# Kernel optimization log

Hardware: AMD Instinct MI355X
Metric: run time of the kernel (lower is better)

The kernel has to match this reference:

```python
import jax, jax.numpy as jnp
import numpy as np

B, T, DIM = 1, 1024, 1024
H = 8
QLR, KVLR = 768, 512
DNOPE, DROPE, DV = 128, 64, 128
DK = DNOPE + DROPE  # 192
EPS = 1e-5


def _rms(x, w):
    return x * jax.lax.rsqrt(jnp.mean(x * x, axis=-1, keepdims=True) + EPS) * w


def _l2norm(x):
    return x * jax.lax.rsqrt(jnp.sum(x * x, axis=-1, keepdims=True) + 1e-6)


def setup_inputs() -> dict:
    key = jax.random.key(0)
    ks = jax.random.split(key, 12)
    std = 0.02
    rnd = lambda k, shape: (jax.random.normal(k, shape, dtype=jnp.float32) * std)
    return {
        'x': jax.random.normal(ks[0], (B, T, DIM), dtype=jnp.float32),
        'cos': jax.random.normal(ks[1], (T, DROPE), dtype=jnp.float32),
        'sin': jax.random.normal(ks[2], (T, DROPE), dtype=jnp.float32),
        'wq_a': rnd(ks[3], (DIM, QLR)),
        'q_norm_w': jnp.ones((QLR,), dtype=jnp.float32),
        'wq_b': rnd(ks[4], (QLR, H * DK)),
        'wkv_a': rnd(ks[5], (DIM, KVLR + DROPE)),
        'kv_norm_w': jnp.ones((KVLR,), dtype=jnp.float32),
        'wkv_b': rnd(ks[6], (KVLR, H * (DNOPE + DV))),
        'wg_w': rnd(ks[7], (DIM, H * DK)),
        'wg_b': jnp.zeros((H * DK,), dtype=jnp.float32),
        'wb': rnd(ks[8], (DIM, H)),
        'wo': rnd(ks[9], (H * DV, DIM)),
    }


def _kda(q, k, v, g, beta):
    # q,k: [B,T,H,DK]; v: [B,T,H,DV]; g: [B,T,H,DK] (log-decay); beta: [B,T,H]
    q = _l2norm(q) * (DK ** -0.5)
    k = _l2norm(k)
    # time-major for scan
    qs = jnp.moveaxis(q, 1, 0)
    ks_ = jnp.moveaxis(k, 1, 0)
    vs = jnp.moveaxis(v, 1, 0)
    gs = jnp.moveaxis(g, 1, 0)
    bs = jnp.moveaxis(beta, 1, 0)

    def step(S, inp):
        q_t, k_t, v_t, g_t, b_t = inp  # [B,H,DK],[B,H,DK],[B,H,DV],[B,H,DK],[B,H]
        S = S * jnp.exp(g_t)[..., None]                       # per-key-dim decay
        u_t = b_t[..., None] * (v_t - jnp.einsum('bhk,bhkv->bhv', k_t, S))
        S = S + k_t[..., None] * u_t[..., None, :]            # rank-1 delta update
        o_t = jnp.einsum('bhk,bhkv->bhv', q_t, S)
        return S, o_t

    S0 = jnp.zeros((B, H, DK, DV), dtype=q.dtype)
    _, o = jax.lax.scan(step, S0, (qs, ks_, vs, gs, bs))
    return jnp.moveaxis(o, 0, 1)  # [B,T,H,DV]


def reference(x, cos, sin, wq_a, q_norm_w, wq_b, wkv_a, kv_norm_w, wkv_b, wg_w, wg_b, wb, wo):
    # cos/sin are accepted but unused, matching the original forward body.
    q = (_rms(x @ wq_a, q_norm_w) @ wq_b).reshape(B, T, H, DK)
    kv_all = x @ wkv_a
    kv_c, k_pe = kv_all[..., :KVLR], kv_all[..., KVLR:]       # [B,T,KVLR],[B,T,DROPE]
    kv = (_rms(kv_c, kv_norm_w) @ wkv_b).reshape(B, T, H, DNOPE + DV)
    k_nope, v = kv[..., :DNOPE], kv[..., DNOPE:]
    k = jnp.concatenate(
        [k_nope, jnp.broadcast_to(k_pe[:, :, None, :], (B, T, H, DROPE))], axis=-1)
    g = jax.nn.log_sigmoid(x @ wg_w + wg_b).reshape(B, T, H, DK)
    beta = jax.nn.sigmoid(x @ wb).reshape(B, T, H)
    o = _kda(q, k, v, g, beta)
    o = jnp.nan_to_num(o, nan=0.0, posinf=10000.0, neginf=-10000.0)
    return o.reshape(B, T, H * DV) @ wo
```

## Files before the change

kernel.cpp:

```cpp
#include <hip/hip_runtime.h>
#include <hip/hip_bf16.h>
#include <math.h>

#define TT 1024
#define DIM 1024
#define HH 8
#define QLR 768
#define KVLR 512
#define DNOPE 128
#define DROPE 64
#define DV 128
#define DK 192
#define HDK (HH*DK)
#define HKV (HH*(DNOPE+DV))
#define NBODY (TT/16)

#define OY   0
#define OQ   3072
#define OC   6144
#define OPL  9984
#define OU   10240
#define OLAM 12288
#define OGY  12480
#define OGQ  12736
#define PABLK 12992

typedef __attribute__((ext_vector_type(8))) short short8;
typedef __attribute__((ext_vector_type(4))) float f32x4;

__device__ __forceinline__ unsigned short f2bf_rn(float f) {
    unsigned u = __float_as_uint(f);
    unsigned lsb = (u >> 16) & 1u;
    u += 0x7fffu + lsb;
    return (unsigned short)(u >> 16);
}
__device__ __forceinline__ float bf2f(unsigned short h) {
    return __uint_as_float(((unsigned)h) << 16);
}

__global__ __launch_bounds__(256) void wconv(
    const float* __restrict__ W0, unsigned short* __restrict__ H0,
    unsigned short* __restrict__ L0, int K0, int N0, int T0,
    const float* __restrict__ W1, unsigned short* __restrict__ H1,
    unsigned short* __restrict__ L1, int K1, int N1, int T1,
    const float* __restrict__ W2, unsigned short* __restrict__ H2,
    unsigned short* __restrict__ L2, int K2, int N2, int T2)
{
    __shared__ float Ls[64][65];
    int bx = blockIdx.x;
    const float* W; unsigned short* H; unsigned short* L; int K, N;
    if (bx < T0)           { W = W0; H = H0; L = L0; K = K0; N = N0; }
    else if (bx < T0 + T1) { bx -= T0; W = W1; H = H1; L = L1; K = K1; N = N1; }
    else                   { bx -= T0 + T1; W = W2; H = H2; L = L2; K = K2; N = N2; }

    const int NT = N >> 6;
    const int kt = bx / NT, nt = bx - kt * NT;
    const int k0 = kt * 64, n0 = nt * 64;
    const int tid = threadIdx.x;
    const int r = tid >> 2, c = (tid & 3) * 16;

#pragma unroll
    for (int i = 0; i < 4; i++)
        *(float4*)&Ls[r][c + i * 4] =
            *(const float4*)&W[(size_t)(k0 + r) * N + n0 + c + i * 4];
    __syncthreads();

    const int nr = tid >> 2, kc = (tid & 3) * 16;
    unsigned short hb[16], lb[16];
#pragma unroll
    for (int j = 0; j < 16; j++) {
        float v = Ls[kc + j][nr];
        unsigned short h = f2bf_rn(v);
        hb[j] = h;
        lb[j] = f2bf_rn(v - bf2f(h));
    }
    size_t ob = (size_t)(n0 + nr) * K + k0 + kc;
    *(float4*)&H[ob]     = ((float4*)hb)[0];
    *(float4*)&H[ob + 8] = ((float4*)hb)[1];
    *(float4*)&L[ob]     = ((float4*)lb)[0];
    *(float4*)&L[ob + 8] = ((float4*)lb)[1];
}

__global__ __launch_bounds__(256) void aconv(
    const float* __restrict__ A, unsigned short* __restrict__ H,
    unsigned short* __restrict__ L)
{
    int i = (blockIdx.x * 256 + threadIdx.x) * 8;
    float4 v0 = *(const float4*)&A[i];
    float4 v1 = *(const float4*)&A[i + 4];
    float vv[8] = {v0.x, v0.y, v0.z, v0.w, v1.x, v1.y, v1.z, v1.w};
    unsigned short hb[8], lb[8];
#pragma unroll
    for (int j = 0; j < 8; j++) {
        unsigned short h = f2bf_rn(vv[j]);
        hb[j] = h;
        lb[j] = f2bf_rn(vv[j] - bf2f(h));
    }
    *(float4*)&H[i] = *(float4*)hb;
    *(float4*)&L[i] = *(float4*)lb;
}

__global__ __launch_bounds__(128) void gemm_bt(
    const unsigned short* __restrict__ Ah0, const unsigned short* __restrict__ Al0,
    const unsigned short* __restrict__ Bh0, const unsigned short* __restrict__ Bl0,
    float* __restrict__ C0, int K0, int N0, int T0,
    const unsigned short* __restrict__ Ah1, const unsigned short* __restrict__ Al1,
    const unsigned short* __restrict__ Bh1, const unsigned short* __restrict__ Bl1,
    float* __restrict__ C1, int K1, int N1, int T1,
    const unsigned short* __restrict__ Ah2, const unsigned short* __restrict__ Al2,
    const unsigned short* __restrict__ Bh2, const unsigned short* __restrict__ Bl2,
    float* __restrict__ C2, int K2, int N2, int T2)
{
    __shared__ unsigned short Ahs[64 * 40], Als[64 * 40];
    __shared__ unsigned short Bhs[64 * 40], Bls[64 * 40];

    int bx = blockIdx.x;
    const unsigned short *Ah, *Al, *Bh, *Bl; float* C; int K, N;
    if (bx < T0) {
        Ah = Ah0; Al = Al0; Bh = Bh0; Bl = Bl0; C = C0; K = K0; N = N0;
    } else if (bx < T0 + T1) {
        bx -= T0; Ah = Ah1; Al = Al1; Bh = Bh1; Bl = Bl1; C = C1; K = K1; N = N1;
    } else {
        bx -= T0 + T1; Ah = Ah2; Al = Al2; Bh = Bh2; Bl = Bl2; C = C2; K = K2; N = N2;
    }

    const int tid = threadIdx.x;
    const int w = tid >> 6, l = tid & 63;
    const int q = l >> 4, m16 = l & 15;
    const int bm = blockIdx.y * 64, bn = bx * 64;

    const int c0i = tid * 2, c1i = tid * 2 + 1;
    const int r0 = c0i >> 2, o0 = (c0i & 3) * 8;
    const int r1 = c1i >> 2, o1 = (c1i & 3) * 8;
    const unsigned short* pAh0 = Ah + (size_t)(bm + r0) * K + o0;
    const unsigned short* pAh1 = Ah + (size_t)(bm + r1) * K + o1;
    const unsigned short* pAl0 = Al + (size_t)(bm + r0) * K + o0;
    const unsigned short* pAl1 = Al + (size_t)(bm + r1) * K + o1;
    const unsigned short* pBh0 = Bh + (size_t)(bn + r0) * K + o0;
    const unsigned short* pBh1 = Bh + (size_t)(bn + r1) * K + o1;
    const unsigned short* pBl0 = Bl + (size_t)(bn + r0) * K + o0;
    const unsigned short* pBl1 = Bl + (size_t)(bn + r1) * K + o1;

    f32x4 acc[2][4];
#pragma unroll
    for (int i = 0; i < 2; i++)
#pragma unroll
        for (int j = 0; j < 4; j++)
            acc[i][j] = (f32x4){0.f, 0.f, 0.f, 0.f};

    float4 vAh0 = *(const float4*)pAh0, vAh1 = *(const float4*)pAh1;
    float4 vAl0 = *(const float4*)pAl0, vAl1 = *(const float4*)pAl1;
    float4 vBh0 = *(const float4*)pBh0, vBh1 = *(const float4*)pBh1;
    float4 vBl0 = *(const float4*)pBl0, vBl1 = *(const float4*)pBl1;

    for (int k0 = 0;; k0 += 32) {
        __syncthreads();
        *(float4*)&Ahs[r0 * 40 + o0] = vAh0; *(float4*)&Ahs[r1 * 40 + o1] = vAh1;
        *(float4*)&Als[r0 * 40 + o0] = vAl0; *(float4*)&Als[r1 * 40 + o1] = vAl1;
        *(float4*)&Bhs[r0 * 40 + o0] = vBh0; *(float4*)&Bhs[r1 * 40 + o1] = vBh1;
        *(float4*)&Bls[r0 * 40 + o0] = vBl0; *(float4*)&Bls[r1 * 40 + o1] = vBl1;
        __syncthreads();

        const bool more = (k0 + 32) < K;
        if (more) {
            const int kn = k0 + 32;
            vAh0 = *(const float4*)(pAh0 + kn); vAh1 = *(const float4*)(pAh1 + kn);
            vAl0 = *(const float4*)(pAl0 + kn); vAl1 = *(const float4*)(pAl1 + kn);
            vBh0 = *(const float4*)(pBh0 + kn); vBh1 = *(const float4*)(pBh1 + kn);
            vBl0 = *(const float4*)(pBl0 + kn); vBl1 = *(const float4*)(pBl1 + kn);
        }

        short8 fah[2], fal[2], fbh[4], fbl[4];
#pragma unroll
        for (int mt = 0; mt < 2; mt++) {
            const int row = w * 32 + mt * 16 + m16;
            fah[mt] = *(const short8*)&Ahs[row * 40 + q * 8];
            fal[mt] = *(const short8*)&Als[row * 40 + q * 8];
        }
#pragma unroll
        for (int nt = 0; nt < 4; nt++) {
            const int row = nt * 16 + m16;
            fbh[nt] = *(const short8*)&Bhs[row * 40 + q * 8];
            fbl[nt] = *(const short8*)&Bls[row * 40 + q * 8];
        }
#pragma unroll
        for (int mt = 0; mt < 2; mt++)
#pragma unroll
            for (int nt = 0; nt < 4; nt++) {
                acc[mt][nt] = __builtin_amdgcn_mfma_f32_16x16x32_bf16(
                    fah[mt], fbh[nt], acc[mt][nt], 0, 0, 0);
                acc[mt][nt] = __builtin_amdgcn_mfma_f32_16x16x32_bf16(
                    fah[mt], fbl[nt], acc[mt][nt], 0, 0, 0);
                acc[mt][nt] = __builtin_amdgcn_mfma_f32_16x16x32_bf16(
                    fal[mt], fbh[nt], acc[mt][nt], 0, 0, 0);
            }
        if (!more) break;
    }

#pragma unroll
    for (int mt = 0; mt < 2; mt++)
#pragma unroll
        for (int nt = 0; nt < 4; nt++) {
            const int mrow = bm + w * 32 + mt * 16 + q * 4;
            const int ncol = bn + nt * 16 + m16;
#pragma unroll
            for (int r = 0; r < 4; r++)
                C[(size_t)(mrow + r) * N + ncol] = acc[mt][nt][r];
        }
}

__global__ __launch_bounds__(256) void rmsnorm_bf2(
    const float* __restrict__ in0, const float* __restrict__ w0,
    unsigned short* __restrict__ oh0, unsigned short* __restrict__ ol0,
    const float* __restrict__ in1, const float* __restrict__ w1,
    unsigned short* __restrict__ oh1, unsigned short* __restrict__ ol1)
{
    int bx = blockIdx.x;
    const float* in; const float* w; unsigned short *oh, *ol;
    int t, stride, ncols; float inv_n;
    if (bx < TT) {
        t = bx; in = in0; w = w0; oh = oh0; ol = ol0;
        stride = QLR; ncols = QLR; inv_n = 1.f / QLR;
    } else {
        t = bx - TT; in = in1; w = w1; oh = oh1; ol = ol1;
        stride = KVLR + DROPE; ncols = KVLR; inv_n = 1.f / KVLR;
    }
    const int tid = threadIdx.x;
    const float* row = in + (size_t)t * stride;
    float ss = 0.f;
    for (int c = tid; c < ncols; c += 256) { float v = row[c]; ss += v * v; }
#pragma unroll
    for (int m = 1; m < 64; m <<= 1) ss += __shfl_xor(ss, m);
    __shared__ float red[4];
    if ((tid & 63) == 0) red[tid >> 6] = ss;
    __syncthreads();
    float tot = red[0] + red[1] + red[2] + red[3];
    float scale = rsqrtf(tot * inv_n + 1e-5f);
    for (int c = tid; c < ncols; c += 256) {
        float v = row[c] * scale * w[c];
        unsigned short h = f2bf_rn(v);
        oh[(size_t)t * ncols + c] = h;
        ol[(size_t)t * ncols + c] = f2bf_rn(v - bf2f(h));
    }
}

__global__ __launch_bounds__(256) void small_fused(
    const float* __restrict__ g, const float* __restrict__ bias,
    float* __restrict__ la_h,
    const float* __restrict__ x, const float* __restrict__ wb,
    float* __restrict__ betab,
    const float* __restrict__ qraw, const float* __restrict__ kvb,
    const float* __restrict__ kv_all, float* __restrict__ q_h,
    float* __restrict__ k_h)
{
    int bx = blockIdx.x;
    if (bx < 6144) {
        int i = bx * 256 + threadIdx.x;
        int t = i / HDK, col = i - t * HDK;
        int h = col / DK, d = col - h * DK;
        float z = g[i] + bias[col];
        float la = fminf(z, 0.f) - log1pf(__expf(-fabsf(z)));
        la_h[((size_t)h * TT + t) * DK + d] = la;
        return;
    }
    bx -= 6144;
    const int lane = threadIdx.x & 63, wv = threadIdx.x >> 6;
    if (bx < 2048) {
        const int p = bx * 4 + wv;
        const int t = p >> 3, h = p & 7;
        const float* xr = x + (size_t)t * DIM;
        float s = 0.f;
        for (int e = lane; e < DIM; e += 64) s += xr[e] * wb[e * HH + h];
#pragma unroll
        for (int m = 1; m < 64; m <<= 1) s += __shfl_xor(s, m);
        if (lane == 0) betab[p] = 1.f / (1.f + expf(-s));
        return;
    }
    bx -= 2048;
    {
        const int p = bx * 4 + wv;
        const int t = p >> 3, h = p & 7;

        const float* qrow = qraw + (size_t)t * HDK + h * DK;
        float q0 = qrow[lane], q1 = qrow[lane + 64], q2 = qrow[lane + 128];
        float ss = q0 * q0 + q1 * q1 + q2 * q2;
#pragma unroll
        for (int m = 1; m < 64; m <<= 1) ss += __shfl_xor(ss, m);
        float sc = rsqrtf(ss + 1e-6f) * 0.07216878364870323f;
        float* qo = q_h + ((size_t)h * TT + t) * DK;
        qo[lane] = q0 * sc; qo[lane + 64] = q1 * sc; qo[lane + 128] = q2 * sc;

        const float* knope = kvb + (size_t)t * HKV + h * (DNOPE + DV);
        float k0 = knope[lane], k1 = knope[lane + 64];
        float k2 = kv_all[(size_t)t * (KVLR + DROPE) + KVLR + lane];
        float ks = k0 * k0 + k1 * k1 + k2 * k2;
#pragma unroll
        for (int m = 1; m < 64; m <<= 1) ks += __shfl_xor(ks, m);
        float kc = rsqrtf(ks + 1e-6f);
        float* ko = k_h + ((size_t)h * TT + t) * DK;
        ko[lane] = k0 * kc; ko[lane + 64] = k1 * kc; ko[lane + 128] = k2 * kc;
    }
}

__device__ __forceinline__ float dpp_xor1(float x) {
    return __int_as_float(__builtin_amdgcn_update_dpp(
        0, __float_as_int(x), 0xB1, 0xF, 0xF, false));
}
__device__ __forceinline__ float dpp_xor2(float x) {
    return __int_as_float(__builtin_amdgcn_update_dpp(
        0, __float_as_int(x), 0x4E, 0xF, 0xF, false));
}
__device__ __forceinline__ float dpp_hm(float x) {
    return __int_as_float(__builtin_amdgcn_update_dpp(
        0, __float_as_int(x), 0x141, 0xF, 0xF, false));
}
__device__ __forceinline__ float red16(float x) {
    x += dpp_xor1(x);
    x += dpp_xor2(x);
    x += dpp_hm(x);
    x += __int_as_float(__builtin_amdgcn_update_dpp(0, __float_as_int(x), 0x140, 0xF, 0xF, false));
    return x;
}

__device__ __forceinline__ void gl_lds16(const float* g, float* l) {
    __builtin_amdgcn_global_load_lds(
        (const __attribute__((address_space(1))) void*)g,
        (__attribute__((address_space(3))) void*)l, 16, 0, 0);
}

__global__ __launch_bounds__(256) void chunk_prep(
    const float* __restrict__ k_h, const float* __restrict__ la_h,
    const float* __restrict__ q_h, const float* __restrict__ kvb,
    const float* __restrict__ betab, float* __restrict__ pa)
{
    __shared__ float Ls[16][196];
    __shared__ float Ks[16][196];
    __shared__ float Qs[16][196];
    __shared__ float Ws[16][196];
    __shared__ float Xs[16][196];
    __shared__ float Ms[16][16];
    __shared__ float bs[16];

    const int tid = threadIdx.x;
    const int n = blockIdx.x >> 3, h = blockIdx.x & 7;
    const size_t g0 = ((size_t)h * TT + n * 16) * DK;
    float* blob = pa + (size_t)blockIdx.x * PABLK;

#pragma unroll
    for (int s = 0; s < 3; s++) {
        int off = (tid * 3 + s) * 4;
        int r = off / 192, c = off - r * 192;
        *(float4*)&Ks[r][c] = *(const float4*)(k_h + g0 + off);
        *(float4*)&Ls[r][c] = *(const float4*)(la_h + g0 + off);
        *(float4*)&Qs[r][c] = *(const float4*)(q_h + g0 + off);
    }
    if (tid < 16) bs[tid] = betab[(size_t)(n * 16 + tid) * HH + h];
    __syncthreads();

    if (tid < 192) {
        float g = 0.f;
#pragma unroll
        for (int i = 0; i < 16; i++) { g += Ls[i][tid]; Ls[i][tid] = g; }
    }
    __syncthreads();

#pragma unroll
    for (int s = 0; s < 12; s++) {
        int idx = s * 256 + tid;
        int i = idx / 192, d = idx - i * 192;
        float G = Ls[i][d];
        float eg = __expf(G), en = __expf(-G);
        float kk = Ks[i][d];
        Ws[i][d] = bs[i] * kk * eg;
        Qs[i][d] *= eg;
        Ks[i][d] = kk * en;
    }
    __syncthreads();

#pragma unroll
    for (int s = 0; s < 3; s++) {
        int off = (tid * 3 + s) * 4;
        int r = off / 192, c = off - r * 192;
        *(float4*)(blob + OQ + off) = *(const float4*)&Qs[r][c];
    }
    if (tid < 192) {
        float lam = __expf(Ls[15][tid]);
        blob[OLAM + tid] = lam;
#pragma unroll
        for (int j4 = 0; j4 < 4; j4++) {
            float4 v;
            v.x = Ks[j4 * 4 + 0][tid] * lam; v.y = Ks[j4 * 4 + 1][tid] * lam;
            v.z = Ks[j4 * 4 + 2][tid] * lam; v.w = Ks[j4 * 4 + 3][tid] * lam;
            *(float4*)(blob + OC + tid * 20 + j4 * 4) = v;
        }
        blob[OC + tid * 20 + 16] = lam;
        blob[OC + tid * 20 + 17] = 0.f;
        blob[OC + tid * 20 + 18] = 0.f; blob[OC + tid * 20 + 19] = 0.f;
    }
    {
        const int i = tid >> 4, j = tid & 15;
        float m = 0.f, p = 0.f;
#pragma unroll
        for (int d4 = 0; d4 < 48; d4++) {
            float4 w  = *(const float4*)&Ws[i][d4 * 4];
            float4 ka = *(const float4*)&Ks[j][d4 * 4];
            float4 qa = *(const float4*)&Qs[i][d4 * 4];
            m += w.x * ka.x + w.y * ka.y + w.z * ka.z + w.w * ka.w;
            p += qa.x * ka.x + qa.y * ka.y + qa.z * ka.z + qa.w * ka.w;
        }
        Ms[i][j] = (j < i) ? m : 0.f;
        blob[OPL + tid] = (j <= i) ? p : 0.f;
    }
    __syncthreads();

    float y[16], uu[16];
    const bool doY = (tid < 192);
    const bool doU = (tid >= 128);
    const int dcol = tid, ccol = tid - 128;
    if (doY) {
#pragma unroll
        for (int i = 0; i < 16; i++) y[i] = Ws[i][dcol];
#pragma unroll
        for (int i = 1; i < 16; i++)
#pragma unroll
            for (int j = 0; j < i; j++)
                y[i] = fmaf(-Ms[i][j], y[j], y[i]);
    }
    if (doU) {
#pragma unroll
        for (int i = 0; i < 16; i++)
            uu[i] = bs[i] * kvb[(size_t)(n * 16 + i) * HKV + h * (DNOPE + DV) + DNOPE + ccol];
#pragma unroll
        for (int i = 1; i < 16; i++)
#pragma unroll
            for (int j = 0; j < i; j++)
                uu[i] = fmaf(-Ms[i][j], uu[j], uu[i]);
    }
    if (doY) {
#pragma unroll
        for (int i = 0; i < 16; i++) Xs[i][dcol] = y[i];
    }
    __syncthreads();
#pragma unroll
    for (int s = 0; s < 3; s++) {
        int off = (tid * 3 + s) * 4;
        int r = off / 192, c = off - r * 192;
        *(float4*)(blob + OY + off) = *(const float4*)&Xs[r][c];
    }
    if (doU) {
#pragma unroll
        for (int i4 = 0; i4 < 4; i4++) {
            float4 t;
            t.x = uu[i4 * 4 + 0]; t.y = uu[i4 * 4 + 1];
            t.z = uu[i4 * 4 + 2]; t.w = uu[i4 * 4 + 3];
            *(float4*)(blob + OU + (size_t)ccol * 16 + i4 * 4) = t;
        }
    }
}

__global__ __launch_bounds__(256) void chunk_prep2(float* __restrict__ pa)
{
    __shared__ float Kcs[16][204];
    __shared__ float Ys[16][200];
    __shared__ float Qs[16][200];
    __shared__ float lamp[192];

    const int tid = threadIdx.x;
    const int n = blockIdx.x >> 3, h = blockIdx.x & 7;
    float* blob = pa + (size_t)blockIdx.x * PABLK;
    if (n == 0) {
        blob[OGY + tid] = 0.f;
        blob[OGQ + tid] = 0.f;
        return;
    }
    const float* pblob = pa + (size_t)((n - 1) * 8 + h) * PABLK;
    if (tid < 192) {
        lamp[tid] = pblob[OLAM + tid];
        float4 a  = *(const float4*)(pblob + OC + tid * 20);
        float4 b  = *(const float4*)(pblob + OC + tid * 20 + 4);
        float4 c  = *(const float4*)(pblob + OC + tid * 20 + 8);
        float4 d4 = *(const float4*)(pblob + OC + tid * 20 + 12);
        Kcs[0][tid]  = a.x;  Kcs[1][tid]  = a.y;  Kcs[2][tid]  = a.z;  Kcs[3][tid]  = a.w;
        Kcs[4][tid]  = b.x;  Kcs[5][tid]  = b.y;  Kcs[6][tid]  = b.z;  Kcs[7][tid]  = b.w;
        Kcs[8][tid]  = c.x;  Kcs[9][tid]  = c.y;  Kcs[10][tid] = c.z;  Kcs[11][tid] = c.w;
        Kcs[12][tid] = d4.x; Kcs[13][tid] = d4.y; Kcs[14][tid] = d4.z; Kcs[15][tid] = d4.w;
    }
#pragma unroll
    for (int s = 0; s < 3; s++) {
        int off = (tid * 3 + s) * 4;
        int r = off / 192, c2 = off - r * 192;
        *(float4*)&Ys[r][c2] = *(const float4*)(blob + OY + off);
        *(float4*)&Qs[r][c2] = *(const float4*)(blob + OQ + off);
    }
    __syncthreads();

    const int i = tid >> 4, j = tid & 15;
    float gy0 = 0.f, gy1 = 0.f, gq0 = 0.f, gq1 = 0.f;
#pragma unroll
    for (int d4 = 0; d4 < 48; d4++) {
        float4 kv = *(const float4*)&Kcs[j][d4 * 4];
        float4 yv = *(const float4*)&Ys[i][d4 * 4];
        float4 qv = *(const float4*)&Qs[i][d4 * 4];
        gy0 = fmaf(yv.x, kv.x, gy0); gy1 = fmaf(yv.y, kv.y, gy1);
        gy0 = fmaf(yv.z, kv.z, gy0); gy1 = fmaf(yv.w, kv.w, gy1);
        gq0 = fmaf(qv.x, kv.x, gq0); gq1 = fmaf(qv.y, kv.y, gq1);
        gq0 = fmaf(qv.z, kv.z, gq0); gq1 = fmaf(qv.w, kv.w, gq1);
    }
    blob[OGY + tid] = gy0 + gy1;
    blob[OGQ + tid] = gq0 + gq1;

#pragma unroll
    for (int s = 0; s < 3; s++) {
        int off = (tid * 3 + s) * 4;
        int r = off / 192, c2 = off - r * 192;
        float4 yv = *(const float4*)&Ys[r][c2];
        float4 qv = *(const float4*)&Qs[r][c2];
        float4 lv = *(const float4*)&lamp[c2];
        yv.x *= lv.x; yv.y *= lv.y; yv.z *= lv.z; yv.w *= lv.w;
        qv.x *= lv.x; qv.y *= lv.y; qv.z *= lv.z; qv.w *= lv.w;
        *(float4*)(blob + OY + off) = yv;
        *(float4*)(blob + OQ + off) = qv;
    }
}

__global__ __launch_bounds__(1024) void kda_chunk(
    const float* __restrict__ pa, unsigned short* __restrict__ obh,
    unsigned short* __restrict__ obl)
{
    __shared__ float Cb[4][3840];
    __shared__ float Pb[4][256];
    __shared__ float Gyb[4][256];
    __shared__ float Gqb[4][256];
    __shared__ float ubs[4][64];
    __shared__ float lbs[4][192];
    __shared__ float Ss[2][4][200];
    __shared__ float us[2][64];

    const int tid = threadIdx.x;
    const int w = tid >> 6, lane = tid & 63;
    const int h = blockIdx.x & 7, cg = blockIdx.x >> 3;
    const int c0 = cg * 4;

    const int ti = w;
    const int cc = lane >> 4;
    const int dg = lane & 15;
    const int dbase = dg * 12;

    auto stage = [&](int buf, int n) {
        const float* blob = pa + (size_t)(n * 8 + h) * PABLK;
        if (w < 15) {
            gl_lds16(blob + OC + w * 256 + lane * 4, &Cb[buf][w * 256]);
            if (w == 0) {
                gl_lds16(blob + OGY + lane * 4, &Gyb[buf][0]);
            } else if (w == 1) {
                gl_lds16(blob + OGQ + lane * 4, &Gqb[buf][0]);
            } else if (w == 2) {
                if (lane < 16)
                    gl_lds16(blob + OU + c0 * 16 + lane * 4, &ubs[buf][0]);
            } else if (w == 3) {
                if (lane < 48)
                    gl_lds16(blob + OLAM + lane * 4, &lbs[buf][0]);
            }
        } else {
            gl_lds16(blob + OPL + lane * 4, &Pb[buf][0]);
        }
    };

    auto ldYQ = [&](int n, float4 (&Y)[3], float4 (&Q)[3]) {
        const float* blob = pa + (size_t)(n * 8 + h) * PABLK;
        const float* py_ = blob + OY + ti * 192 + dbase;
        const float* pq_ = blob + OQ + ti * 192 + dbase;
#pragma unroll
        for (int s = 0; s < 3; s++) {
            Y[s] = *(const float4*)(py_ + s * 4);
            Q[s] = *(const float4*)(pq_ + s * 4);
        }
    };

    auto body = [&](int n, float4 (&Yc)[3], float4 (&Qc)[3], float& zqc) {
        const int p = n & 1, q = p ^ 1;
        const int bn = n & 3, bp = (n - 1) & 3;

        const float* Sp = &Ss[q][cc][dbase];
        float4 sv0 = *(const float4*)Sp;
        float4 sv1 = *(const float4*)(Sp + 4);
        float4 sv2 = *(const float4*)(Sp + 8);
        float upv = us[q][cc * 16 + dg];
        float gyv = Gyb[bn][ti * 16 + dg];
        float gqv = Gqb[bn][ti * 16 + dg];
        float ubv = ubs[bn][cc * 16 + ti];

        float py0 = gyv * upv, py1 = 0.f;
        float pq0 = gqv * upv, pq1 = 0.f;
        py0 = fmaf(Yc[0].x, sv0.x, py0); py1 = fmaf(Yc[0].y, sv0.y, py1);
        py0 = fmaf(Yc[0].z, sv0.z, py0); py1 = fmaf(Yc[0].w, sv0.w, py1);
        pq0 = fmaf(Qc[0].x, sv0.x, pq0); pq1 = fmaf(Qc[0].y, sv0.y, pq1);
        pq0 = fmaf(Qc[0].z, sv0.z, pq0); pq1 = fmaf(Qc[0].w, sv0.w, pq1);
        py0 = fmaf(Yc[1].x, sv1.x, py0); py1 = fmaf(Yc[1].y, sv1.y, py1);
        py0 = fmaf(Yc[1].z, sv1.z, py0); py1 = fmaf(Yc[1].w, sv1.w, py1);
        pq0 = fmaf(Qc[1].x, sv1.x, pq0); pq1 = fmaf(Qc[1].y, sv1.y, pq1);
        pq0 = fmaf(Qc[1].z, sv1.z, pq0); pq1 = fmaf(Qc[1].w, sv1.w, pq1);
        py0 = fmaf(Yc[2].x, sv2.x, py0); py1 = fmaf(Yc[2].y, sv2.y, py1);
        py0 = fmaf(Yc[2].z, sv2.z, py0); py1 = fmaf(Yc[2].w, sv2.w, py1);
        pq0 = fmaf(Qc[2].x, sv2.x, pq0); pq1 = fmaf(Qc[2].y, sv2.y, pq1);
        pq0 = fmaf(Qc[2].z, sv2.z, pq0); pq1 = fmaf(Qc[2].w, sv2.w, pq1);

        float zy = red16(py0 + py1);
        float zq = red16(pq0 + pq1);
        if (dg == 0) us[p][cc * 16 + ti] = ubv - zy;

        if (n > 0) {
            float oa = red16((dg <= ti) ? Pb[bp][ti * 16 + dg] * upv : 0.f);
            if (dg == 0) {
                float ov = zqc + oa;
                if (isnan(ov)) ov = 0.f;
                else if (isinf(ov)) ov = ov > 0.f ? 1e4f : -1e4f;
                size_t oi = (size_t)((n - 1) * 16 + ti) * (HH * DV) + h * DV + c0 + cc;
                unsigned short hb = f2bf_rn(ov);
                obh[oi] = hb;
                obl[oi] = f2bf_rn(ov - bf2f(hb));
            }
            if (tid < 768) {
                const int d = tid >> 2, c = tid & 3;
                float sprev = Ss[q][c][d];
                const float4* U4 = (const float4*)&us[q][c * 16];
                float4 u0 = U4[0], u1 = U4[1], u2v = U4[2], u3 = U4[3];
                const float4* C4 = (const float4*)&Cb[bp][d * 20];
                float4 k0 = C4[0], k1 = C4[1], k2 = C4[2], k3 = C4[3];
                float a0 = lbs[bp][d] * sprev, a1 = 0.f;
                a0 = fmaf(k0.x, u0.x,  a0); a1 = fmaf(k0.y, u0.y,  a1);
                a0 = fmaf(k0.z, u0.z,  a0); a1 = fmaf(k0.w, u0.w,  a1);
                a0 = fmaf(k1.x, u1.x,  a0); a1 = fmaf(k1.y, u1.y,  a1);
                a0 = fmaf(k1.z, u1.z,  a0); a1 = fmaf(k1.w, u1.w,  a1);
                a0 = fmaf(k2.x, u2v.x, a0); a1 = fmaf(k2.y, u2v.y, a1);
                a0 = fmaf(k2.z, u2v.z, a0); a1 = fmaf(k2.w, u2v.w, a1);
                a0 = fmaf(k3.x, u3.x,  a0); a1 = fmaf(k3.y, u3.y,  a1);
                a0 = fmaf(k3.z, u3.z,  a0); a1 = fmaf(k3.w, u3.w,  a1);
                Ss[p][c][d] = a0 + a1;
            }
        }
        zqc = zq;
    };

#define SEG_BAR asm volatile("s_waitcnt lgkmcnt(0)\n\ts_barrier" ::: "memory")

    for (int i = tid; i < 1600; i += 1024) ((float*)Ss)[i] = 0.f;
    if (tid < 128) ((float*)us)[tid] = 0.f;
    stage(0, 0);
    stage(1, 1);
    asm volatile("" ::: "memory");
    float4 Ya[3], Qa[3], Yb[3], Qb[3];
    ldYQ(0, Ya, Qa);
    float zqc = 0.f;
    asm volatile("s_waitcnt vmcnt(0) lgkmcnt(0)\n\ts_barrier" ::: "memory");

    for (int n = 0; n < NBODY; n += 2) {
        if (n + 2 < NBODY) stage((n + 2) & 3, n + 2);
        asm volatile("" ::: "memory");
        ldYQ(n + 1, Yb, Qb);
        body(n, Ya, Qa, zqc);
        SEG_BAR;
        if (n + 3 < NBODY) stage((n + 3) & 3, n + 3);
        asm volatile("" ::: "memory");
        if (n + 2 < NBODY) ldYQ(n + 2, Ya, Qa);
        body(n + 1, Yb, Qb, zqc);
        SEG_BAR;
    }
    {
        float upv = us[1][cc * 16 + dg];
        float oa = red16((dg <= ti) ? Pb[(NBODY - 1) & 3][ti * 16 + dg] * upv : 0.f);
        if (dg == 0) {
            float ov = zqc + oa;
            if (isnan(ov)) ov = 0.f;
            else if (isinf(ov)) ov = ov > 0.f ? 1e4f : -1e4f;
            size_t oi = (size_t)((NBODY - 1) * 16 + ti) * (HH * DV) + h * DV + c0 + cc;
            unsigned short hb = f2bf_rn(ov);
            obh[oi] = hb;
            obl[oi] = f2bf_rn(ov - bf2f(hb));
        }
    }
#undef SEG_BAR
}

extern "C" void kernel_launch(void* const* d_in, const int* in_sizes, int n_in,
                              void* d_out, int out_size, void* d_ws, size_t ws_size,
                              hipStream_t stream)
{
    const float* x         = (const float*)d_in[0];
    const float* wq_a      = (const float*)d_in[3];
    const float* q_norm_w  = (const float*)d_in[4];
    const float* wq_b      = (const float*)d_in[5];
    const float* wkv_a     = (const float*)d_in[6];
    const float* kv_norm_w = (const float*)d_in[7];
    const float* wkv_b     = (const float*)d_in[8];
    const float* wg_w      = (const float*)d_in[9];
    const float* wg_b      = (const float*)d_in[10];
    const float* wb        = (const float*)d_in[11];
    const float* wo        = (const float*)d_in[12];
    float* out = (float*)d_out;

    float* ws = (float*)d_ws;
    float* xq     = ws;
    float* kv_all = xq     + TT * QLR;
    float* agraw  = kv_all + TT * (KVLR + DROPE);
    float* qnraw  = agraw  + TT * HDK;
    float* kvb    = qnraw  + TT * HDK;
    float* la_h   = kvb    + TT * HKV;
    float* q_h    = la_h   + TT * HDK;
    float* k_h    = q_h    + TT * HDK;
    float* betab  = k_h    + TT * HDK;
    float* pa     = betab  + TT * HH;
    float* tail   = pa     + 512 * PABLK;

    unsigned short* wo_h  = (unsigned short*)tail;
    unsigned short* wo_l  = wo_h  + 1048576;
    unsigned short* xh    = wo_l  + 1048576;
    unsigned short* xl    = xh    + 1048576;
    unsigned short* xqh   = xl    + 1048576;
    unsigned short* xql   = xqh   + 786432;
    unsigned short* kvnh  = xql   + 786432;
    unsigned short* kvnl  = kvnh  + 524288;

    unsigned short* wqa_h  = (unsigned short*)pa;
    unsigned short* wqa_l  = wqa_h  + 786432;
    unsigned short* wkva_h = wqa_l  + 786432;
    unsigned short* wkva_l = wkva_h + 589824;
    unsigned short* wgw_h  = wkva_l + 589824;
    unsigned short* wgw_l  = wgw_h  + 1572864;
    unsigned short* wqb_h  = wgw_l  + 1572864;
    unsigned short* wqb_l  = wqb_h  + 1179648;
    unsigned short* wkvb_h = wqb_l  + 1179648;
    unsigned short* wkvb_l = wkvb_h + 1048576;

    unsigned short* obh = (unsigned short*)agraw;
    unsigned short* obl = obh + 1048576;

    dim3 blk(256);

    wconv<<<dim3(192 + 144 + 384), blk, 0, stream>>>(
        wq_a, wqa_h, wqa_l, DIM, QLR, 192,
        wkv_a, wkva_h, wkva_l, DIM, KVLR + DROPE, 144,
        wg_w, wgw_h, wgw_l, DIM, HDK, 384);
    wconv<<<dim3(288 + 256 + 256), blk, 0, stream>>>(
        wq_b, wqb_h, wqb_l, QLR, HDK, 288,
        wkv_b, wkvb_h, wkvb_l, KVLR, HKV, 256,
        wo, wo_h, wo_l, DIM, DIM, 256);

    aconv<<<dim3(TT * DIM / (256 * 8)), blk, 0, stream>>>(x, xh, xl);

    gemm_bt<<<dim3(12 + 9 + 24, 16), dim3(128), 0, stream>>>(
        xh, xl, wqa_h, wqa_l, xq, DIM, QLR, 12,
        xh, xl, wkva_h, wkva_l, kv_all, DIM, KVLR + DROPE, 9,
        xh, xl, wgw_h, wgw_l, agraw, DIM, HDK, 24);

    rmsnorm_bf2<<<dim3(2 * TT), blk, 0, stream>>>(
        xq, q_norm_w, xqh, xql,
        kv_all, kv_norm_w, kvnh, kvnl);

    gemm_bt<<<dim3(24 + 32, 16), dim3(128), 0, stream>>>(
        xqh, xql, wqb_h, wqb_l, qnraw, QLR, HDK, 24,
        kvnh, kvnl, wkvb_h, wkvb_l, kvb, KVLR, HKV, 32,
        xh, xl, wqa_h, wqa_l, xq, DIM, QLR, 0);

    small_fused<<<dim3(6144 + 2048 + 2048), blk, 0, stream>>>(
        agraw, wg_b, la_h,
        x, wb, betab,
        qnraw, kvb, kv_all, q_h, k_h);

    chunk_prep<<<512, blk, 0, stream>>>(k_h, la_h, q_h, kvb, betab, pa);
    chunk_prep2<<<512, blk, 0, stream>>>(pa);
    kda_chunk<<<256, dim3(1024), 0, stream>>>(pa, obh, obl);

    gemm_bt<<<dim3(16, 16), dim3(128), 0, stream>>>(
        obh, obl, wo_h, wo_l, out, DIM, DIM, 16,
        xh, xl, wqa_h, wqa_l, xq, DIM, QLR, 0,
        xh, xl, wqa_h, wqa_l, xq, DIM, QLR, 0);
}
```

Baseline: 320.5 us.

## Split recurrent chunk kernel into 512 blocks of 2 value columns with triple buffering

Halves the number of value columns each kda_chunk block handles (2 instead of 4), doubling the grid to 512 blocks of 512 threads. Staging drops from four buffers to three, with a one-chunk prefetch distance instead of two. The aim is more parallel blocks across CUs and a smaller per-block barrier scope on the serial recurrence. In exchange, the C/P/G blobs are fetched twice as often overall and the shallower prefetch may expose more memory latency.

New measurement: 326.3 us. Within noise of the previous version (+1.8%).

```diff
diff --git a/kernel.cpp b/kernel.cpp
--- a/kernel.cpp
+++ b/kernel.cpp
@@ -523,45 +523,47 @@
     }
 }
 
-__global__ __launch_bounds__(1024) void kda_chunk(
+__global__ __launch_bounds__(512) void kda_chunk(
     const float* __restrict__ pa, unsigned short* __restrict__ obh,
     unsigned short* __restrict__ obl)
 {
-    __shared__ float Cb[4][3840];
-    __shared__ float Pb[4][256];
-    __shared__ float Gyb[4][256];
-    __shared__ float Gqb[4][256];
-    __shared__ float ubs[4][64];
-    __shared__ float lbs[4][192];
-    __shared__ float Ss[2][4][200];
-    __shared__ float us[2][64];
+    __shared__ float Cb[3][3840];
+    __shared__ float Pb[3][256];
+    __shared__ float Gyb[3][256];
+    __shared__ float Gqb[3][256];
+    __shared__ float ubs[3][32];
+    __shared__ float lbs[3][192];
+    __shared__ float Ss[2][2][200];
+    __shared__ float us[2][32];
 
     const int tid = threadIdx.x;
     const int w = tid >> 6, lane = tid & 63;
     const int h = blockIdx.x & 7, cg = blockIdx.x >> 3;
-    const int c0 = cg * 4;
-
-    const int ti = w;
-    const int cc = lane >> 4;
+    const int c0 = cg * 2;
+
+    const int ti = (w << 1) | (lane >> 5);
+    const int cc = (lane >> 4) & 1;
     const int dg = lane & 15;
     const int dbase = dg * 12;
 
     auto stage = [&](int buf, int n) {
         const float* blob = pa + (size_t)(n * 8 + h) * PABLK;
-        if (w < 15) {
-            gl_lds16(blob + OC + w * 256 + lane * 4, &Cb[buf][w * 256]);
+        if (w < 7) {
+            gl_lds16(blob + OC + (w * 2) * 256 + lane * 4, &Cb[buf][(w * 2) * 256]);
+            gl_lds16(blob + OC + (w * 2 + 1) * 256 + lane * 4, &Cb[buf][(w * 2 + 1) * 256]);
             if (w == 0) {
                 gl_lds16(blob + OGY + lane * 4, &Gyb[buf][0]);
             } else if (w == 1) {
                 gl_lds16(blob + OGQ + lane * 4, &Gqb[buf][0]);
             } else if (w == 2) {
-                if (lane < 16)
+                if (lane < 8)
                     gl_lds16(blob + OU + c0 * 16 + lane * 4, &ubs[buf][0]);
             } else if (w == 3) {
                 if (lane < 48)
                     gl_lds16(blob + OLAM + lane * 4, &lbs[buf][0]);
             }
         } else {
+            gl_lds16(blob + OC + 14 * 256 + lane * 4, &Cb[buf][14 * 256]);
             gl_lds16(blob + OPL + lane * 4, &Pb[buf][0]);
         }
     };
@@ -577,9 +579,9 @@
         }
     };
 
-    auto body = [&](int n, float4 (&Yc)[3], float4 (&Qc)[3], float& zqc) {
+    auto body = [&](int n, int bn, int bp, float4 (&Yc)[3], float4 (&Qc)[3],
+                    float& zqc) {
         const int p = n & 1, q = p ^ 1;
-        const int bn = n & 3, bp = (n - 1) & 3;
 
         const float* Sp = &Ss[q][cc][dbase];
         float4 sv0 = *(const float4*)Sp;
@@ -620,8 +622,8 @@
                 obh[oi] = hb;
                 obl[oi] = f2bf_rn(ov - bf2f(hb));
             }
-            if (tid < 768) {
-                const int d = tid >> 2, c = tid & 3;
+            if (tid < 384) {
+                const int d = tid >> 1, c = tid & 1;
                 float sprev = Ss[q][c][d];
                 const float4* U4 = (const float4*)&us[q][c * 16];
                 float4 u0 = U4[0], u1 = U4[1], u2v = U4[2], u3 = U4[3];
@@ -644,31 +646,36 @@
 
 #define SEG_BAR asm volatile("s_waitcnt lgkmcnt(0)\n\ts_barrier" ::: "memory")
 
-    for (int i = tid; i < 1600; i += 1024) ((float*)Ss)[i] = 0.f;
-    if (tid < 128) ((float*)us)[tid] = 0.f;
+    for (int i = tid; i < 800; i += 512) ((float*)Ss)[i] = 0.f;
+    if (tid < 64) ((float*)us)[tid] = 0.f;
     stage(0, 0);
-    stage(1, 1);
     asm volatile("" ::: "memory");
     float4 Ya[3], Qa[3], Yb[3], Qb[3];
     ldYQ(0, Ya, Qa);
     float zqc = 0.f;
     asm volatile("s_waitcnt vmcnt(0) lgkmcnt(0)\n\ts_barrier" ::: "memory");
 
+    int b0 = 0;
     for (int n = 0; n < NBODY; n += 2) {
-        if (n + 2 < NBODY) stage((n + 2) & 3, n + 2);
+        int b1 = b0 + 1; if (b1 >= 3) b1 -= 3;
+        int b2 = b1 + 1; if (b2 >= 3) b2 -= 3;
+        stage(b1, n + 1);
         asm volatile("" ::: "memory");
         ldYQ(n + 1, Yb, Qb);
-        body(n, Ya, Qa, zqc);
+        body(n, b0, b2, Ya, Qa, zqc);
         SEG_BAR;
-        if (n + 3 < NBODY) stage((n + 3) & 3, n + 3);
-        asm volatile("" ::: "memory");
-        if (n + 2 < NBODY) ldYQ(n + 2, Ya, Qa);
-        body(n + 1, Yb, Qb, zqc);
+        if (n + 2 < NBODY) {
+            stage(b2, n + 2);
+            asm volatile("" ::: "memory");
+            ldYQ(n + 2, Ya, Qa);
+        }
+        body(n + 1, b1, b0, Yb, Qb, zqc);
         SEG_BAR;
+        b0 = b2;
     }
     {
-        float upv = us[1][cc * 16 + dg];
-        float oa = red16((dg <= ti) ? Pb[(NBODY - 1) & 3][ti * 16 + dg] * upv : 0.f);
+        float upv = us[(NBODY - 1) & 1][cc * 16 + dg];
+        float oa = red16((dg <= ti) ? Pb[(NBODY - 1) % 3][ti * 16 + dg] * upv : 0.f);
         if (dg == 0) {
             float ov = zqc + oa;
             if (isnan(ov)) ov = 0.f;
@@ -769,7 +776,7 @@
 
     chunk_prep<<<512, blk, 0, stream>>>(k_h, la_h, q_h, kvb, betab, pa);
     chunk_prep2<<<512, blk, 0, stream>>>(pa);
-    kda_chunk<<<256, dim3(1024), 0, stream>>>(pa, obh, obl);
+    kda_chunk<<<512, dim3(512), 0, stream>>>(pa, obh, obl);
 
     gemm_bt<<<dim3(16, 16), dim3(128), 0, stream>>>(
         obh, obl, wo_h, wo_l, out, DIM, DIM, 16,
```

## Load GEMM tiles via direct global-to-LDS with XOR swizzle and 128-row tiles

Applied to the files above, without the earlier changes.

The bf16-split GEMM now stages A and B tiles through global_load_lds instead of register loads followed by LDS stores. It uses an XOR-swizzled unpadded LDS layout to avoid bank conflicts, and doubles the M tile to 128 rows with 256 threads so each B tile is reused by four waves. The change is meant to cut register staging and VGPR pressure and to improve B reuse. In exchange it drops the register prefetch of the next k-slice, so loads no longer overlap the MFMA work, and it halves the number of blocks in the grid.

Measured after the change: 332.2 us. 3.6% more time.

```diff
diff --git a/kernel.cpp b/kernel.cpp
--- a/kernel.cpp
+++ b/kernel.cpp
@@ -38,6 +38,17 @@
     return __uint_as_float(((unsigned)h) << 16);
 }
 
+__device__ __forceinline__ void gl_lds16(const float* g, float* l) {
+    __builtin_amdgcn_global_load_lds(
+        (const __attribute__((address_space(1))) void*)g,
+        (__attribute__((address_space(3))) void*)l, 16, 0, 0);
+}
+__device__ __forceinline__ void gl_lds16s(const unsigned short* g, unsigned short* l) {
+    __builtin_amdgcn_global_load_lds(
+        (const __attribute__((address_space(1))) void*)g,
+        (__attribute__((address_space(3))) void*)l, 16, 0, 0);
+}
+
 __global__ __launch_bounds__(256) void wconv(
     const float* __restrict__ W0, unsigned short* __restrict__ H0,
     unsigned short* __restrict__ L0, int K0, int N0, int T0,
@@ -100,7 +111,7 @@
     *(float4*)&L[i] = *(float4*)lb;
 }
 
-__global__ __launch_bounds__(128) void gemm_bt(
+__global__ __launch_bounds__(256) void gemm_bt(
     const unsigned short* __restrict__ Ah0, const unsigned short* __restrict__ Al0,
     const unsigned short* __restrict__ Bh0, const unsigned short* __restrict__ Bl0,
     float* __restrict__ C0, int K0, int N0, int T0,
@@ -111,8 +122,8 @@
     const unsigned short* __restrict__ Bh2, const unsigned short* __restrict__ Bl2,
     float* __restrict__ C2, int K2, int N2, int T2)
 {
-    __shared__ unsigned short Ahs[64 * 40], Als[64 * 40];
-    __shared__ unsigned short Bhs[64 * 40], Bls[64 * 40];
+    __shared__ unsigned short Ahs[128 * 32], Als[128 * 32];
+    __shared__ unsigned short Bhs[64 * 32],  Bls[64 * 32];
 
     int bx = blockIdx.x;
     const unsigned short *Ah, *Al, *Bh, *Bl; float* C; int K, N;
@@ -127,19 +138,9 @@
     const int tid = threadIdx.x;
     const int w = tid >> 6, l = tid & 63;
     const int q = l >> 4, m16 = l & 15;
-    const int bm = blockIdx.y * 64, bn = bx * 64;
-
-    const int c0i = tid * 2, c1i = tid * 2 + 1;
-    const int r0 = c0i >> 2, o0 = (c0i & 3) * 8;
-    const int r1 = c1i >> 2, o1 = (c1i & 3) * 8;
-    const unsigned short* pAh0 = Ah + (size_t)(bm + r0) * K + o0;
-    const unsigned short* pAh1 = Ah + (size_t)(bm + r1) * K + o1;
-    const unsigned short* pAl0 = Al + (size_t)(bm + r0) * K + o0;
-    const unsigned short* pAl1 = Al + (size_t)(bm + r1) * K + o1;
-    const unsigned short* pBh0 = Bh + (size_t)(bn + r0) * K + o0;
-    const unsigned short* pBh1 = Bh + (size_t)(bn + r1) * K + o1;
-    const unsigned short* pBl0 = Bl + (size_t)(bn + r0) * K + o0;
-    const unsigned short* pBl1 = Bl + (size_t)(bn + r1) * K + o1;
+    const int bm = blockIdx.y * 128, bn = bx * 64;
+
+    const int lr = l >> 2, lq = l & 3;
 
     f32x4 acc[2][4];
 #pragma unroll
@@ -148,40 +149,39 @@
         for (int j = 0; j < 4; j++)
             acc[i][j] = (f32x4){0.f, 0.f, 0.f, 0.f};
 
-    float4 vAh0 = *(const float4*)pAh0, vAh1 = *(const float4*)pAh1;
-    float4 vAl0 = *(const float4*)pAl0, vAl1 = *(const float4*)pAl1;
-    float4 vBh0 = *(const float4*)pBh0, vBh1 = *(const float4*)pBh1;
-    float4 vBl0 = *(const float4*)pBl0, vBl1 = *(const float4*)pBl1;
-
-    for (int k0 = 0;; k0 += 32) {
+    for (int k0 = 0; k0 < K; k0 += 32) {
         __syncthreads();
-        *(float4*)&Ahs[r0 * 40 + o0] = vAh0; *(float4*)&Ahs[r1 * 40 + o1] = vAh1;
-        *(float4*)&Als[r0 * 40 + o0] = vAl0; *(float4*)&Als[r1 * 40 + o1] = vAl1;
-        *(float4*)&Bhs[r0 * 40 + o0] = vBh0; *(float4*)&Bhs[r1 * 40 + o1] = vBh1;
-        *(float4*)&Bls[r0 * 40 + o0] = vBl0; *(float4*)&Bls[r1 * 40 + o1] = vBl1;
+#pragma unroll
+        for (int i = 0; i < 2; i++) {
+            const int row = w * 32 + i * 16 + lr;
+            const int qq = lq ^ ((row >> 1) & 3);
+            const size_t go = (size_t)(bm + row) * K + k0 + qq * 8;
+            gl_lds16s(Ah + go, &Ahs[(w * 32 + i * 16) * 32]);
+            gl_lds16s(Al + go, &Als[(w * 32 + i * 16) * 32]);
+        }
+        {
+            const int row = w * 16 + lr;
+            const int qq = lq ^ ((row >> 1) & 3);
+            const size_t go = (size_t)(bn + row) * K + k0 + qq * 8;
+            gl_lds16s(Bh + go, &Bhs[(w * 16) * 32]);
+            gl_lds16s(Bl + go, &Bls[(w * 16) * 32]);
+        }
         __syncthreads();
-
-        const bool more = (k0 + 32) < K;
-        if (more) {
-            const int kn = k0 + 32;
-            vAh0 = *(const float4*)(pAh0 + kn); vAh1 = *(const float4*)(pAh1 + kn);
-            vAl0 = *(const float4*)(pAl0 + kn); vAl1 = *(const float4*)(pAl1 + kn);
-            vBh0 = *(const float4*)(pBh0 + kn); vBh1 = *(const float4*)(pBh1 + kn);
-            vBl0 = *(const float4*)(pBl0 + kn); vBl1 = *(const float4*)(pBl1 + kn);
-        }
 
         short8 fah[2], fal[2], fbh[4], fbl[4];
 #pragma unroll
         for (int mt = 0; mt < 2; mt++) {
             const int row = w * 32 + mt * 16 + m16;
-            fah[mt] = *(const short8*)&Ahs[row * 40 + q * 8];
-            fal[mt] = *(const short8*)&Als[row * 40 + q * 8];
+            const int qa = (q ^ ((row >> 1) & 3)) * 8;
+            fah[mt] = *(const short8*)&Ahs[row * 32 + qa];
+            fal[mt] = *(const short8*)&Als[row * 32 + qa];
         }
 #pragma unroll
         for (int nt = 0; nt < 4; nt++) {
             const int row = nt * 16 + m16;
-            fbh[nt] = *(const short8*)&Bhs[row * 40 + q * 8];
-            fbl[nt] = *(const short8*)&Bls[row * 40 + q * 8];
+            const int qb = (q ^ ((row >> 1) & 3)) * 8;
+            fbh[nt] = *(const short8*)&Bhs[row * 32 + qb];
+            fbl[nt] = *(const short8*)&Bls[row * 32 + qb];
         }
 #pragma unroll
         for (int mt = 0; mt < 2; mt++)
@@ -194,7 +194,6 @@
                 acc[mt][nt] = __builtin_amdgcn_mfma_f32_16x16x32_bf16(
                     fal[mt], fbh[nt], acc[mt][nt], 0, 0, 0);
             }
-        if (!more) break;
     }
 
 #pragma unroll
@@ -320,12 +319,6 @@
     x += dpp_hm(x);
     x += __int_as_float(__builtin_amdgcn_update_dpp(0, __float_as_int(x), 0x140, 0xF, 0xF, false));
     return x;
-}
-
-__device__ __forceinline__ void gl_lds16(const float* g, float* l) {
-    __builtin_amdgcn_global_load_lds(
-        (const __attribute__((address_space(1))) void*)g,
-        (__attribute__((address_space(3))) void*)l, 16, 0, 0);
 }
 
 __global__ __launch_bounds__(256) void chunk_prep(
@@ -748,7 +741,7 @@
 
     aconv<<<dim3(TT * DIM / (256 * 8)), blk, 0, stream>>>(x, xh, xl);
 
-    gemm_bt<<<dim3(12 + 9 + 24, 16), dim3(128), 0, stream>>>(
+    gemm_bt<<<dim3(12 + 9 + 24, 8), dim3(256), 0, stream>>>(
         xh, xl, wqa_h, wqa_l, xq, DIM, QLR, 12,
         xh, xl, wkva_h, wkva_l, kv_all, DIM, KVLR + DROPE, 9,
         xh, xl, wgw_h, wgw_l, agraw, DIM, HDK, 24);
@@ -757,7 +750,7 @@
         xq, q_norm_w, xqh, xql,
         kv_all, kv_norm_w, kvnh, kvnl);
 
-    gemm_bt<<<dim3(24 + 32, 16), dim3(128), 0, stream>>>(
+    gemm_bt<<<dim3(24 + 32, 8), dim3(256), 0, stream>>>(
         xqh, xql, wqb_h, wqb_l, qnraw, QLR, HDK, 24,
         kvnh, kvnl, wkvb_h, wkvb_l, kvb, KVLR, HKV, 32,
         xh, xl, wqa_h, wqa_l, xq, DIM, QLR, 0);
@@ -771,7 +764,7 @@
     chunk_prep2<<<512, blk, 0, stream>>>(pa);
     kda_chunk<<<256, dim3(1024), 0, stream>>>(pa, obh, obl);
 
-    gemm_bt<<<dim3(16, 16), dim3(128), 0, stream>>>(
+    gemm_bt<<<dim3(16, 8), dim3(256), 0, stream>>>(
         obh, obl, wo_h, wo_l, out, DIM, DIM, 16,
         xh, xl, wqa_h, wqa_l, xq, DIM, QLR, 0,
         xh, xl, wqa_h, wqa_l, xq, DIM, QLR, 0);
```
